# Optimization experiments

Measured on AMD Instinct MI355X. Metric: run time of the kernel, lower is better.

The kernel has to match this reference:

```python
import jax, jax.numpy as jnp
import numpy as np

N, E, NNZ = 50000, 10000, 250000   # nodes, hyperedges, incidences
IN_CH, H, D = 128, 64, 6           # in_channels, MLP_hidden, stalk dim
EPS = 1e-5


def setup_inputs() -> dict:
    key = jax.random.key(0)
    ks = jax.random.split(key, 12)
    inp = {}
    inp["x"] = jax.random.normal(ks[0], (N, IN_CH), jnp.float32)
    inp["hyperedge_attr"] = jax.random.normal(ks[1], (E, IN_CH), jnp.float32)  # init_hedge='rand'
    inp["node_idx"] = jax.random.randint(ks[2], (NNZ,), 0, N)
    inp["edge_idx"] = jax.random.randint(ks[3], (NNZ,), 0, E)
    inp["node_types"] = jax.random.randint(ks[4], (N,), 0, 3)
    inp["hyperedge_types"] = jax.random.randint(ks[5], (E,), 0, 6)
    s = 1.0 / np.sqrt(IN_CH)
    inp["W_lin"] = jax.random.uniform(ks[6], (IN_CH, H * D), jnp.float32, -s, s)
    inp["b_lin"] = jnp.zeros((H * D,), jnp.float32)
    inp["ln_g"] = jnp.ones((2 * H,), jnp.float32)
    inp["ln_b"] = jnp.zeros((2 * H,), jnp.float32)
    s2 = 1.0 / np.sqrt(2 * H)
    inp["W_sheaf"] = jax.random.uniform(ks[7], (2 * H, D), jnp.float32, -s2, s2)
    inp["b_sheaf"] = jnp.zeros((D,), jnp.float32)
    s3 = 1.0 / np.sqrt(H)
    inp["W_conv0"] = jax.random.uniform(ks[8], (H, H), jnp.float32, -s3, s3)
    inp["b_conv0"] = jnp.zeros((H,), jnp.float32)
    inp["W_conv1"] = jax.random.uniform(ks[9], (H, H), jnp.float32, -s3, s3)
    inp["b_conv1"] = jnp.zeros((H,), jnp.float32)
    return inp


def _layernorm(x, g, b):
    mu = x.mean(-1, keepdims=True)
    var = ((x - mu) ** 2).mean(-1, keepdims=True)
    return (x - mu) * jax.lax.rsqrt(var + EPS) * g + b


def reference(x, hyperedge_attr, node_idx, edge_idx, node_types, hyperedge_types,
              W_lin, b_lin, ln_g, ln_b, W_sheaf, b_sheaf,
              W_conv0, b_conv0, W_conv1, b_conv1):
    # --- input projection + stalk reshape (self.lin) ---
    xs = (x @ W_lin + b_lin).reshape(N * D, H)              # [N*d, H]
    es = (hyperedge_attr @ W_lin + b_lin).reshape(E * D, H)  # [E*d, H]

    # --- SheafBuilderDiag (local_concat, sigmoid act) ---
    xa = xs.reshape(N, D, H).mean(1)   # [N, H] stalk-averaged node feats
    ea = es.reshape(E, D, H).mean(1)   # [E, H]
    feat = jnp.concatenate([xa[node_idx], ea[edge_idx]], axis=-1)  # [NNZ, 2H]
    alpha = jax.nn.sigmoid(_layernorm(feat, ln_g, ln_b) @ W_sheaf + b_sheaf)  # [NNZ, D]

    dr = jnp.arange(D)
    row_exp = (node_idx[:, None] * D + dr).reshape(-1)  # [NNZ*D] expanded node index
    col_exp = (edge_idx[:, None] * D + dr).reshape(-1)  # [NNZ*D] expanded hyperedge index
    a = alpha.reshape(-1)                               # [NNZ*D]

    # --- degree_norm: D^-1 (nodes) and B^-1 (hyperedges) from incidence counts ---
    ones = jnp.ones_like(a)
    Dn = jax.ops.segment_sum(ones, row_exp, num_segments=N * D)
    Dinv = jnp.where(Dn > 0, 1.0 / Dn, 0.0)
    Bn = jax.ops.segment_sum(ones, col_exp, num_segments=E * D)
    Binv = jnp.where(Bn > 0, 1.0 / Bn, 0.0)

    def conv(xin, W, bias):
        # HyperDiffusionDiagSheafConv: out = xW - D^-1 H^T B^-1 H (xW) + bias
        xl = xin @ W
        m = Binv[:, None] * jax.ops.segment_sum(a[:, None] * xl[row_exp], col_exp, num_segments=E * D)
        agg = Dinv[:, None] * jax.ops.segment_sum(a[:, None] * m[col_exp], row_exp, num_segments=N * D)
        return xl - agg + bias

    h1 = jax.nn.elu(conv(xs, W_conv0, b_conv0))   # dropout inactive (eval)
    h2 = conv(h1, W_conv1, b_conv1)
    return jax.nn.elu(h2.reshape(N, H * D))
```

## Files before the change

### kernel.cpp

```cpp
#include <hip/hip_runtime.h>
#include <hip/hip_bf16.h>

#define N_NODES 50000
#define N_EDGES 10000
#define NNZV    250000
#define IN_CH   128
#define HDIM    64
#define DSTALK  6
#define HD      384
#define NROWS   (N_NODES * DSTALK)
#define EROWS   (N_EDGES * DSTALK)

__global__ __launch_bounds__(256) void k_wefft(
    const float* __restrict__ W_lin, const float* __restrict__ W0,
    float* __restrict__ W0effT) {
  int idx = blockIdx.x * blockDim.x + threadIdx.x;
  if (idx >= IN_CH * HD) return;
  int k = idx / HD, j = idx - k * HD;
  int r = j >> 6, h = j & 63;
  float s = 0.f;
#pragma unroll 8
  for (int m = 0; m < HDIM; m++)
    s += W_lin[k * HD + r * HDIM + m] * W0[m * HDIM + h];
  W0effT[(size_t)j * IN_CH + k] = s;
}

#define WS_BASE (IN_CH * HDIM + HD + HDIM)
#define WS_END  (WS_BASE + 780 + HDIM * HDIM)
__global__ __launch_bounds__(256) void k_wsmall(
    const float* __restrict__ W_lin, const float* __restrict__ b_lin,
    const float* __restrict__ W0, const float* __restrict__ W1,
    const float* __restrict__ g, const float* __restrict__ bln,
    const float* __restrict__ Ws, const float* __restrict__ bs,
    float* __restrict__ Wm, float* __restrict__ cm, float* __restrict__ c0,
    float* __restrict__ gwN, float* __restrict__ gwE,
    float* __restrict__ G, float* __restrict__ K, float* __restrict__ W1T) {
  int idx = blockIdx.x * blockDim.x + threadIdx.x;
  if (idx < IN_CH * HDIM) {
    int k = idx >> 6, h = idx & 63;
    float s = 0.f;
#pragma unroll
    for (int r = 0; r < DSTALK; r++) s += W_lin[k * HD + r * HDIM + h];
    Wm[idx] = s * (1.f / 6.f);
  } else if (idx < IN_CH * HDIM + HD) {
    int j = idx - IN_CH * HDIM;
    int r = j >> 6, h = j & 63;
    float s = 0.f;
#pragma unroll 8
    for (int m = 0; m < HDIM; m++) s += b_lin[r * HDIM + m] * W0[m * HDIM + h];
    c0[j] = s;
  } else if (idx < WS_BASE) {
    int h = idx - IN_CH * HDIM - HD;
    float s = 0.f;
#pragma unroll
    for (int r = 0; r < DSTALK; r++) s += b_lin[r * HDIM + h];
    cm[h] = s * (1.f / 6.f);
  } else if (idx < WS_BASE + 384) {
    int i = idx - WS_BASE;
    int h = i / 6, r = i - h * 6;
    gwN[i] = g[h] * Ws[h * DSTALK + r];
  } else if (idx < WS_BASE + 768) {
    int i = idx - WS_BASE - 384;
    int h = i / 6, r = i - h * 6;
    gwE[i] = g[64 + h] * Ws[(64 + h) * DSTALK + r];
  } else if (idx < WS_BASE + 774) {
    int r = idx - WS_BASE - 768;
    float s = 0.f;
    for (int i = 0; i < 2 * HDIM; i++) s += g[i] * Ws[i * DSTALK + r];
    G[r] = s;
  } else if (idx < WS_BASE + 780) {
    int r = idx - WS_BASE - 774;
    float s = 0.f;
    for (int i = 0; i < 2 * HDIM; i++) s += bln[i] * Ws[i * DSTALK + r];
    K[r] = s + bs[r];
  } else if (idx < WS_END) {
    int i = idx - WS_BASE - 780;
    int c = i >> 6, k = i & 63;
    W1T[c * HDIM + k] = W1[k * HDIM + c];
  }
}

__global__ __launch_bounds__(256) void k_xa_stats(
    const float* __restrict__ x, const float* __restrict__ ea,
    const float* __restrict__ Wm, const float* __restrict__ cm,
    const float* __restrict__ gwN, const float* __restrict__ gwE,
    float* __restrict__ stats) {
  __shared__ float lx[64][IN_CH];
  __shared__ float ox[64][HDIM + 1];
  __shared__ float lgw[2][64 * DSTALK];
  const int row0 = blockIdx.x * 64;
  const int tid = threadIdx.x;
  for (int i = tid; i < 2 * 64 * DSTALK; i += 256) {
    int which = i / 384, k = i - which * 384;
    lgw[which][k] = which ? gwE[k] : gwN[k];
  }
  for (int i = tid; i < 64 * IN_CH; i += 256) {
    int r = i >> 7, k = i & 127;
    int row = row0 + r;
    float v = 0.f;
    if (row < N_NODES) v = x[row * IN_CH + k];
    else if (row < N_NODES + N_EDGES) v = ea[(row - N_NODES) * IN_CH + k];
    lx[r][k] = v;
  }
  __syncthreads();
  const int col = tid & 63, rg = tid >> 6;
  float acc[16];
#pragma unroll
  for (int i = 0; i < 16; i++) acc[i] = 0.f;
  for (int k = 0; k < IN_CH; k++) {
    float w = Wm[k * HDIM + col];
#pragma unroll
    for (int i = 0; i < 16; i++) acc[i] += lx[rg * 16 + i][k] * w;
  }
  const float c = cm[col];
#pragma unroll
  for (int i = 0; i < 16; i++) ox[rg * 16 + i][col] = acc[i] + c;
  __syncthreads();
  for (int t = tid; t < 512; t += 256) {
    int row = t >> 3, st = t & 7;
    int grow = row0 + row;
    if (grow >= N_NODES + N_EDGES) continue;
    const float* __restrict__ gw = (grow >= N_NODES) ? lgw[1] : lgw[0];
    float s = 0.f;
    if (st == 0) {
#pragma unroll 8
      for (int h = 0; h < HDIM; h++) s += ox[row][h];
    } else if (st == 1) {
#pragma unroll 8
      for (int h = 0; h < HDIM; h++) { float v = ox[row][h]; s += v * v; }
    } else {
      int r = st - 2;
#pragma unroll 8
      for (int h = 0; h < HDIM; h++) s += ox[row][h] * gw[h * DSTALK + r];
    }
    stats[(size_t)grow * 8 + st] = s;
  }
}

__global__ __launch_bounds__(256) void k_xl0(
    const float* __restrict__ x, const float* __restrict__ W0effT,
    const float* __restrict__ c0, float* __restrict__ xl0) {
  __shared__ float4 xav[16][65];
  __shared__ float4 wbv[16][65];
  const int tid = threadIdx.x;
  const int row0 = blockIdx.x * 64;
  const int col0 = blockIdx.y * 64;
  const int tc = tid & 15, tr = tid >> 4;
  float acc[4][4] = {{0.f}};
  for (int kc = 0; kc < 2; kc++) {
    if (kc) __syncthreads();
#pragma unroll
    for (int i = 0; i < 4; i++) {
      int fidx = tid + i * 256;
      int row = fidx >> 4, kq = fidx & 15;
      int gk = kc * 64 + kq * 4;
      int grow = row0 + row;
      float4 v = make_float4(0.f, 0.f, 0.f, 0.f);
      if (grow < N_NODES) v = *(const float4*)(x + (size_t)grow * IN_CH + gk);
      xav[kq][row] = v;
      wbv[kq][row] = *(const float4*)(W0effT + (size_t)(col0 + row) * IN_CH + gk);
    }
    __syncthreads();
    for (int kq = 0; kq < 16; kq++) {
      float4 xa[4], wb[4];
#pragma unroll
      for (int i = 0; i < 4; i++) xa[i] = xav[kq][tr + (i << 4)];
#pragma unroll
      for (int j = 0; j < 4; j++) wb[j] = wbv[kq][tc + (j << 4)];
#pragma unroll
      for (int i = 0; i < 4; i++)
#pragma unroll
        for (int j = 0; j < 4; j++)
          acc[i][j] += xa[i].x * wb[j].x + xa[i].y * wb[j].y +
                       xa[i].z * wb[j].z + xa[i].w * wb[j].w;
    }
  }
#pragma unroll
  for (int i = 0; i < 4; i++) {
    int row = row0 + tr + (i << 4);
    if (row >= N_NODES) continue;
#pragma unroll
    for (int j = 0; j < 4; j++) {
      int col = col0 + tc + (j << 4);
      xl0[(size_t)row * HD + col] = acc[i][j] + c0[col];
    }
  }
}

__global__ __launch_bounds__(256) void k_xw(
    const float* __restrict__ xin, const float* __restrict__ W1T,
    float* __restrict__ xl) {
  __shared__ float4 xav[16][65];
  __shared__ float4 wbv[16][65];
  const int tid = threadIdx.x;
  const int row0 = blockIdx.x * 64;
  const int tc = tid & 15, tr = tid >> 4;
#pragma unroll
  for (int i = 0; i < 4; i++) {
    int fidx = tid + i * 256;
    int row = fidx >> 4, kq = fidx & 15;
    int grow = row0 + row;
    float4 v = make_float4(0.f, 0.f, 0.f, 0.f);
    if (grow < NROWS) v = *(const float4*)(xin + (size_t)grow * HDIM + kq * 4);
    xav[kq][row] = v;
    wbv[kq][row] = *(const float4*)(W1T + row * HDIM + kq * 4);
  }
  __syncthreads();
  float acc[4][4] = {{0.f}};
  for (int kq = 0; kq < 16; kq++) {
    float4 xa[4], wb[4];
#pragma unroll
    for (int i = 0; i < 4; i++) xa[i] = xav[kq][tr + (i << 4)];
#pragma unroll
    for (int j = 0; j < 4; j++) wb[j] = wbv[kq][tc + (j << 4)];
#pragma unroll
    for (int i = 0; i < 4; i++)
#pragma unroll
      for (int j = 0; j < 4; j++)
        acc[i][j] += xa[i].x * wb[j].x + xa[i].y * wb[j].y +
                     xa[i].z * wb[j].z + xa[i].w * wb[j].w;
  }
#pragma unroll
  for (int i = 0; i < 4; i++) {
    int row = row0 + tr + (i << 4);
    if (row >= NROWS) continue;
#pragma unroll
    for (int j = 0; j < 4; j++) {
      int col = tc + (j << 4);
      xl[(size_t)row * HDIM + col] = acc[i][j];
    }
  }
}

__global__ __launch_bounds__(256) void k_sheaf2(
    const int* __restrict__ nidx, const int* __restrict__ eidx,
    const float* __restrict__ stats,
    const float* __restrict__ G, const float* __restrict__ K,
    float* __restrict__ alpha) {
  int j = blockIdx.x * blockDim.x + threadIdx.x;
  if (j >= NNZV) return;
  int n = nidx[j], e = eidx[j];
  const float4* __restrict__ sn = (const float4*)(stats + (size_t)n * 8);
  const float4* __restrict__ se = (const float4*)(stats + ((size_t)(N_NODES + e)) * 8);
  float4 a0 = sn[0], a1 = sn[1];
  float4 b0 = se[0], b1 = se[1];
  float mu = (a0.x + b0.x) * (1.f / 128.f);
  float var = (a0.y + b0.y) * (1.f / 128.f) - mu * mu;
  float rs = rsqrtf(var + 1e-5f);
  float p[DSTALK] = {a0.z + b0.z, a0.w + b0.w, a1.x + b1.x,
                     a1.y + b1.y, a1.z + b1.z, a1.w + b1.w};
#pragma unroll
  for (int r = 0; r < DSTALK; r++) {
    float z = rs * (p[r] - mu * G[r]) + K[r];
    alpha[(size_t)j * DSTALK + r] = 1.f / (1.f + expf(-z));
  }
}

__global__ void k_count(const int* __restrict__ nidx, const int* __restrict__ eidx,
                        int* __restrict__ cntN, int* __restrict__ cntE) {
  int j = blockIdx.x * blockDim.x + threadIdx.x;
  if (j < NNZV) {
    atomicAdd(&cntN[nidx[j]], 1);
    atomicAdd(&cntE[eidx[j]], 1);
  }
}

__global__ __launch_bounds__(256) void k_scan_a(
    const int* __restrict__ cnt, int n, int* __restrict__ row,
    int* __restrict__ bsum) {
  const int b = blockIdx.x, t = threadIdx.x;
  const int i0 = b * 512 + 2 * t, i1 = i0 + 1;
  int c0 = (i0 < n) ? cnt[i0] : 0;
  int c1 = (i1 < n) ? cnt[i1] : 0;
  int ts = c0 + c1;
  const int lane = t & 63, wv = t >> 6;
  int s = ts;
#pragma unroll
  for (int o = 1; o < 64; o <<= 1) {
    int v = __shfl_up(s, o);
    if (lane >= o) s += v;
  }
  __shared__ int wsum[4];
  if (lane == 63) wsum[wv] = s;
  __syncthreads();
  int wbase = 0;
#pragma unroll
  for (int wprev = 0; wprev < 3; wprev++)
    if (wprev < wv) wbase += wsum[wprev];
  const int incl = wbase + s;
  const int excl = incl - ts;
  if (i0 < n) row[i0] = excl;
  if (i1 < n) row[i1] = excl + c0;
  if (t == 255) bsum[b] = incl;
}

__global__ __launch_bounds__(128) void k_scan_b(
    const int* __restrict__ bsum, int nb, int* __restrict__ bbase) {
  const int t = threadIdx.x;
  int v = (t < nb) ? bsum[t] : 0;
  const int lane = t & 63, wv = t >> 6;
  int s = v;
#pragma unroll
  for (int o = 1; o < 64; o <<= 1) {
    int u = __shfl_up(s, o);
    if (lane >= o) s += u;
  }
  __shared__ int wsum[2];
  if (lane == 63) wsum[wv] = s;
  __syncthreads();
  const int incl = ((wv == 1) ? wsum[0] : 0) + s;
  if (t < nb) bbase[t] = incl - v;
  if (t == 127) bbase[nb] = incl;
}

__global__ __launch_bounds__(256) void k_scan_c(
    const int* __restrict__ cnt, const int* __restrict__ bbase, int n, int nb,
    int* __restrict__ row, int* __restrict__ fill, float* __restrict__ inv) {
  int i = blockIdx.x * blockDim.x + threadIdx.x;
  if (i < n) {
    int v = row[i] + bbase[i >> 9];
    row[i] = v;
    fill[i] = v;
    int c = cnt[i];
    inv[i] = c > 0 ? 1.f / (float)c : 0.f;
  }
  if (i == 0) row[n] = bbase[nb];
}

__global__ void k_fill(const int* __restrict__ nidx, const int* __restrict__ eidx,
                       int* __restrict__ fillN, int* __restrict__ fillE,
                       int* __restrict__ jlN, int* __restrict__ jlE,
                       int* __restrict__ elN, int* __restrict__ nlE) {
  int j = blockIdx.x * blockDim.x + threadIdx.x;
  if (j < NNZV) {
    int n = nidx[j], e = eidx[j];
    int p = atomicAdd(&fillN[n], 1);
    jlN[p] = j; elN[p] = e;
    int q = atomicAdd(&fillE[e], 1);
    jlE[q] = j; nlE[q] = n;
  }
}

__global__ __launch_bounds__(256) void k_gather_e(
    const int* __restrict__ rowE, const int* __restrict__ jlE,
    const int* __restrict__ nlE, const float* __restrict__ alpha,
    const float* __restrict__ xl, const float* __restrict__ Binv,
    float* __restrict__ msum) {
  int e = (blockIdx.x * blockDim.x + threadIdx.x) >> 6;
  int lane = threadIdx.x & 63;
  if (e >= N_EDGES) return;
  float acc[DSTALK];
#pragma unroll
  for (int r = 0; r < DSTALK; r++) acc[r] = 0.f;
  const int lo = rowE[e], hi = rowE[e + 1];
  for (int p = lo; p < hi; p++) {
    const int j = jlE[p];
    const int n = nlE[p];
    const float* __restrict__ xr = xl + (size_t)n * HD + lane;
    const float* __restrict__ ar = alpha + (size_t)j * DSTALK;
#pragma unroll
    for (int r = 0; r < DSTALK; r++) acc[r] += ar[r] * xr[r * HDIM];
  }
  const float bv = Binv[e];
  float* __restrict__ mr = msum + (size_t)e * HD + lane;
#pragma unroll
  for (int r = 0; r < DSTALK; r++) mr[r * HDIM] = acc[r] * bv;
}

__global__ __launch_bounds__(256) void k_gather_n(
    const int* __restrict__ rowN, const int* __restrict__ jlN,
    const int* __restrict__ elN, const float* __restrict__ alpha,
    const float* __restrict__ msum, const float* __restrict__ Dinv,
    const float* __restrict__ xl, const float* __restrict__ bias,
    float* __restrict__ outp) {
  int n = (blockIdx.x * blockDim.x + threadIdx.x) >> 6;
  int lane = threadIdx.x & 63;
  if (n >= N_NODES) return;
  float acc[DSTALK];
#pragma unroll
  for (int r = 0; r < DSTALK; r++) acc[r] = 0.f;
  const int lo = rowN[n], hi = rowN[n + 1];
  for (int p = lo; p < hi; p++) {
    const int j = jlN[p];
    const int e = elN[p];
    const float* __restrict__ mr = msum + (size_t)e * HD + lane;
    const float* __restrict__ ar = alpha + (size_t)j * DSTALK;
#pragma unroll
    for (int r = 0; r < DSTALK; r++) acc[r] += ar[r] * mr[r * HDIM];
  }
  const float dv = Dinv[n];
  const float bb = bias[lane];
  const float* __restrict__ xr = xl + (size_t)n * HD + lane;
  float* __restrict__ orow = outp + (size_t)n * HD + lane;
#pragma unroll
  for (int r = 0; r < DSTALK; r++) {
    float v = xr[r * HDIM] + bb - dv * acc[r];
    orow[r * HDIM] = v > 0.f ? v : expm1f(v);
  }
}

extern "C" void kernel_launch(void* const* d_in, const int* in_sizes, int n_in,
                              void* d_out, int out_size, void* d_ws, size_t ws_size,
                              hipStream_t stream) {
  const float* x    = (const float*)d_in[0];
  const float* hea  = (const float*)d_in[1];
  const int*  nidx  = (const int*)d_in[2];
  const int*  eidx  = (const int*)d_in[3];
  const float* W_lin = (const float*)d_in[6];
  const float* b_lin = (const float*)d_in[7];
  const float* ln_g  = (const float*)d_in[8];
  const float* ln_b  = (const float*)d_in[9];
  const float* W_sh  = (const float*)d_in[10];
  const float* b_sh  = (const float*)d_in[11];
  const float* W_c0  = (const float*)d_in[12];
  const float* b_c0  = (const float*)d_in[13];
  const float* W_c1  = (const float*)d_in[14];
  const float* b_c1  = (const float*)d_in[15];
  float* out = (float*)d_out;

  char* ws = (char*)d_ws;
  size_t off = 0;
  auto alloc = [&](size_t bytes) {
    size_t o = off;
    off = (off + bytes + 255) & ~(size_t)255;
    return o;
  };
  size_t o_xl0   = alloc((size_t)NROWS * HDIM * 4);
  size_t o_msum  = alloc((size_t)EROWS * HDIM * 4);
  size_t o_alpha = alloc((size_t)NNZV * DSTALK * 4);
  size_t o_stats = alloc((size_t)(N_NODES + N_EDGES) * 8 * 4);
  size_t o_jlN   = alloc((size_t)NNZV * 4);
  size_t o_jlE   = alloc((size_t)NNZV * 4);
  size_t o_elN   = alloc((size_t)NNZV * 4);
  size_t o_nlE   = alloc((size_t)NNZV * 4);
  size_t o_cntN  = alloc((size_t)N_NODES * 4);
  size_t o_cntE  = alloc((size_t)N_EDGES * 4);
  size_t o_rowN  = alloc((size_t)(N_NODES + 1) * 4);
  size_t o_rowE  = alloc((size_t)(N_EDGES + 1) * 4);
  size_t o_filN  = alloc((size_t)N_NODES * 4);
  size_t o_filE  = alloc((size_t)N_EDGES * 4);
  size_t o_Dinv  = alloc((size_t)N_NODES * 4);
  size_t o_Binv  = alloc((size_t)N_EDGES * 4);
  size_t o_bsN   = alloc((size_t)256 * 4);
  size_t o_bbN   = alloc((size_t)256 * 4);
  size_t o_bsE   = alloc((size_t)256 * 4);
  size_t o_bbE   = alloc((size_t)256 * 4);
  size_t o_WeffT = alloc((size_t)IN_CH * HD * 4);
  size_t o_Wm    = alloc((size_t)IN_CH * HDIM * 4);
  size_t o_cm    = alloc((size_t)HDIM * 4);
  size_t o_c0    = alloc((size_t)HD * 4);
  size_t o_gwN   = alloc((size_t)64 * DSTALK * 4);
  size_t o_gwE   = alloc((size_t)64 * DSTALK * 4);
  size_t o_G     = alloc((size_t)DSTALK * 4);
  size_t o_K     = alloc((size_t)DSTALK * 4);
  size_t o_W1T   = alloc((size_t)HDIM * HDIM * 4);

  float* xl0    = (float*)(ws + o_xl0);
  float* msum   = (float*)(ws + o_msum);
  float* alpha  = (float*)(ws + o_alpha);
  float* stats  = (float*)(ws + o_stats);
  int*   jlN    = (int*)(ws + o_jlN);
  int*   jlE    = (int*)(ws + o_jlE);
  int*   elN    = (int*)(ws + o_elN);
  int*   nlE    = (int*)(ws + o_nlE);
  int*   cntN   = (int*)(ws + o_cntN);
  int*   cntE   = (int*)(ws + o_cntE);
  int*   rowN   = (int*)(ws + o_rowN);
  int*   rowE   = (int*)(ws + o_rowE);
  int*   filN   = (int*)(ws + o_filN);
  int*   filE   = (int*)(ws + o_filE);
  float* Dinv   = (float*)(ws + o_Dinv);
  float* Binv   = (float*)(ws + o_Binv);
  int*   bsN    = (int*)(ws + o_bsN);
  int*   bbN    = (int*)(ws + o_bbN);
  int*   bsE    = (int*)(ws + o_bsE);
  int*   bbE    = (int*)(ws + o_bbE);
  float* W0effT = (float*)(ws + o_WeffT);
  float* Wm     = (float*)(ws + o_Wm);
  float* cm     = (float*)(ws + o_cm);
  float* c0     = (float*)(ws + o_c0);
  float* gwN    = (float*)(ws + o_gwN);
  float* gwE    = (float*)(ws + o_gwE);
  float* G      = (float*)(ws + o_G);
  float* K      = (float*)(ws + o_K);
  float* W1T    = (float*)(ws + o_W1T);

  const int NB_N = (N_NODES + 511) / 512;
  const int NB_E = (N_EDGES + 511) / 512;

  k_wefft<<<(IN_CH * HD + 255) / 256, 256, 0, stream>>>(W_lin, W_c0, W0effT);
  k_wsmall<<<(WS_END + 255) / 256, 256, 0, stream>>>(
      W_lin, b_lin, W_c0, W_c1, ln_g, ln_b, W_sh, b_sh,
      Wm, cm, c0, gwN, gwE, G, K, W1T);

  hipMemsetAsync(ws + o_cntN, 0, (size_t)N_NODES * 4, stream);
  hipMemsetAsync(ws + o_cntE, 0, (size_t)N_EDGES * 4, stream);
  k_count<<<(NNZV + 255) / 256, 256, 0, stream>>>(nidx, eidx, cntN, cntE);
  k_scan_a<<<NB_N, 256, 0, stream>>>(cntN, N_NODES, rowN, bsN);
  k_scan_a<<<NB_E, 256, 0, stream>>>(cntE, N_EDGES, rowE, bsE);
  k_scan_b<<<1, 128, 0, stream>>>(bsN, NB_N, bbN);
  k_scan_b<<<1, 128, 0, stream>>>(bsE, NB_E, bbE);
  k_scan_c<<<(N_NODES + 255) / 256, 256, 0, stream>>>(cntN, bbN, N_NODES, NB_N,
                                                      rowN, filN, Dinv);
  k_scan_c<<<(N_EDGES + 255) / 256, 256, 0, stream>>>(cntE, bbE, N_EDGES, NB_E,
                                                      rowE, filE, Binv);
  k_fill<<<(NNZV + 255) / 256, 256, 0, stream>>>(nidx, eidx, filN, filE,
                                                 jlN, jlE, elN, nlE);

  k_xa_stats<<<(N_NODES + N_EDGES + 63) / 64, 256, 0, stream>>>(
      x, hea, Wm, cm, gwN, gwE, stats);

  k_sheaf2<<<(NNZV + 255) / 256, 256, 0, stream>>>(nidx, eidx, stats, G, K, alpha);

  {
    dim3 g((N_NODES + 63) / 64, HD / 64);
    k_xl0<<<g, 256, 0, stream>>>(x, W0effT, c0, xl0);
  }
  k_gather_e<<<(N_EDGES + 3) / 4, 256, 0, stream>>>(rowE, jlE, nlE, alpha, xl0, Binv, msum);
  k_gather_n<<<(N_NODES + 3) / 4, 256, 0, stream>>>(rowN, jlN, elN, alpha, msum, Dinv,
                                                    xl0, b_c0, xl0);

  k_xw<<<(NROWS + 63) / 64, 256, 0, stream>>>(xl0, W1T, xl0);
  k_gather_e<<<(N_EDGES + 3) / 4, 256, 0, stream>>>(rowE, jlE, nlE, alpha, xl0, Binv, msum);
  k_gather_n<<<(N_NODES + 3) / 4, 256, 0, stream>>>(rowN, jlN, elN, alpha, msum, Dinv,
                                                    xl0, b_c1, out);

  (void)in_sizes; (void)n_in; (void)out_size; (void)ws_size;
}
```

Measured before the change: 672.4 us.

## Enlarge k_xl0 GEMM tiles to 128x128 with register-prefetched K stages

The x@W0eff GEMM kernel now uses 128x128 output tiles with an 8x8 per-thread accumulator instead of 64x64 with 4x4. The K dimension is split into four 32-wide chunks, and the next chunk is loaded into registers while the current one is computed from shared memory. The bias values are also hoisted into registers before the store loop. This raises arithmetic intensity and hides global load latency, but it increases register pressure (64 accumulators plus operands), which may lower occupancy, and it launches fewer blocks.

```diff
diff --git a/kernel.cpp b/kernel.cpp
--- a/kernel.cpp
+++ b/kernel.cpp
@@ -140,49 +140,75 @@
 __global__ __launch_bounds__(256) void k_xl0(
     const float* __restrict__ x, const float* __restrict__ W0effT,
     const float* __restrict__ c0, float* __restrict__ xl0) {
-  __shared__ float4 xav[16][65];
-  __shared__ float4 wbv[16][65];
+  __shared__ float4 aS[8][129];
+  __shared__ float4 bS[8][129];
   const int tid = threadIdx.x;
-  const int row0 = blockIdx.x * 64;
-  const int col0 = blockIdx.y * 64;
+  const int row0 = blockIdx.x * 128;
+  const int col0 = blockIdx.y * 128;
   const int tc = tid & 15, tr = tid >> 4;
-  float acc[4][4] = {{0.f}};
-  for (int kc = 0; kc < 2; kc++) {
-    if (kc) __syncthreads();
+  float4 pa[4], pb[4];
+
+#define STAGE_LOAD(kc)                                                        \
+  {                                                                           \
+    _Pragma("unroll")                                                         \
+    for (int i = 0; i < 4; i++) {                                             \
+      int fidx = tid + (i << 8);                                              \
+      int row = fidx >> 3, kq = fidx & 7;                                     \
+      int gk = (kc) * 32 + kq * 4;                                            \
+      int grow = row0 + row;                                                  \
+      pa[i] = (grow < N_NODES)                                                \
+                  ? *(const float4*)(x + (size_t)grow * IN_CH + gk)           \
+                  : make_float4(0.f, 0.f, 0.f, 0.f);                          \
+      pb[i] = *(const float4*)(W0effT + (size_t)(col0 + row) * IN_CH + gk);   \
+    }                                                                         \
+  }
+
+  float acc[8][8];
+#pragma unroll
+  for (int i = 0; i < 8; i++)
+#pragma unroll
+    for (int j = 0; j < 8; j++) acc[i][j] = 0.f;
+
+  STAGE_LOAD(0);
+#pragma unroll 1
+  for (int kc = 0; kc < 4; kc++) {
 #pragma unroll
     for (int i = 0; i < 4; i++) {
-      int fidx = tid + i * 256;
-      int row = fidx >> 4, kq = fidx & 15;
-      int gk = kc * 64 + kq * 4;
-      int grow = row0 + row;
-      float4 v = make_float4(0.f, 0.f, 0.f, 0.f);
-      if (grow < N_NODES) v = *(const float4*)(x + (size_t)grow * IN_CH + gk);
-      xav[kq][row] = v;
-      wbv[kq][row] = *(const float4*)(W0effT + (size_t)(col0 + row) * IN_CH + gk);
+      int fidx = tid + (i << 8);
+      int row = fidx >> 3, kq = fidx & 7;
+      aS[kq][row] = pa[i];
+      bS[kq][row] = pb[i];
     }
     __syncthreads();
-    for (int kq = 0; kq < 16; kq++) {
-      float4 xa[4], wb[4];
-#pragma unroll
-      for (int i = 0; i < 4; i++) xa[i] = xav[kq][tr + (i << 4)];
-#pragma unroll
-      for (int j = 0; j < 4; j++) wb[j] = wbv[kq][tc + (j << 4)];
-#pragma unroll
-      for (int i = 0; i < 4; i++)
-#pragma unroll
-        for (int j = 0; j < 4; j++)
-          acc[i][j] += xa[i].x * wb[j].x + xa[i].y * wb[j].y +
-                       xa[i].z * wb[j].z + xa[i].w * wb[j].w;
+    if (kc < 3) STAGE_LOAD(kc + 1);
+#pragma unroll 2
+    for (int kq = 0; kq < 8; kq++) {
+      float4 a[8];
+#pragma unroll
+      for (int i = 0; i < 8; i++) a[i] = aS[kq][tr + (i << 4)];
+#pragma unroll
+      for (int j = 0; j < 8; j++) {
+        float4 b = bS[kq][tc + (j << 4)];
+#pragma unroll
+        for (int i = 0; i < 8; i++)
+          acc[i][j] += a[i].x * b.x + a[i].y * b.y + a[i].z * b.z + a[i].w * b.w;
+      }
     }
-  }
-#pragma unroll
-  for (int i = 0; i < 4; i++) {
+    __syncthreads();
+  }
+#undef STAGE_LOAD
+
+  float cc[8];
+#pragma unroll
+  for (int j = 0; j < 8; j++) cc[j] = c0[col0 + tc + (j << 4)];
+#pragma unroll
+  for (int i = 0; i < 8; i++) {
     int row = row0 + tr + (i << 4);
     if (row >= N_NODES) continue;
-#pragma unroll
-    for (int j = 0; j < 4; j++) {
-      int col = col0 + tc + (j << 4);
-      xl0[(size_t)row * HD + col] = acc[i][j] + c0[col];
+    float* __restrict__ orow = xl0 + (size_t)row * HD + col0;
+#pragma unroll
+    for (int j = 0; j < 8; j++) {
+      orow[tc + (j << 4)] = acc[i][j] + cc[j];
     }
   }
 }
@@ -513,7 +539,7 @@
   k_sheaf2<<<(NNZV + 255) / 256, 256, 0, stream>>>(nidx, eidx, stats, G, K, alpha);
 
   {
-    dim3 g((N_NODES + 63) / 64, HD / 64);
+    dim3 g((N_NODES + 127) / 128, HD / 128);
     k_xl0<<<g, 256, 0, stream>>>(x, W0effT, c0, xl0);
   }
   k_gather_e<<<(N_EDGES + 3) / 4, 256, 0, stream>>>(rowE, jlE, nlE, alpha, xl0, Binv, msum);
```

New measurement: 697.7 us. 3.8% more time.
